# Kernel optimization log

Hardware: AMD Instinct MI355X
Metric: run time of the kernel (lower is better)

## Reference

```python
import jax, jax.numpy as jnp
import numpy as np

L, B, S, D, H, DK, F = 4, 2, 1024, 1024, 16, 64, 4096
EPS = 1e-5  # torch BatchNorm1d default eps


def setup_inputs() -> dict:
    key = jax.random.key(0)
    ks = iter(jax.random.split(key, 64))
    def nrm(shape, scale=0.02):
        return jax.random.normal(next(ks), shape, dtype=jnp.float32) * scale
    inp = {"x": jax.random.normal(next(ks), (B, S, D), dtype=jnp.float32)}
    for i in (1, 2):  # 1 = masked self-attn, 2 = second (unmasked) self-attn
        inp[f"Wq{i}"] = nrm((L, H, D, DK)); inp[f"bq{i}"] = nrm((L, H, DK))
        inp[f"Wk{i}"] = nrm((L, H, D, DK)); inp[f"bk{i}"] = nrm((L, H, DK))
        inp[f"Wv{i}"] = nrm((L, H, D, DK)); inp[f"bv{i}"] = nrm((L, H, DK))
        inp[f"Wo{i}"] = nrm((L, H * DK, D)); inp[f"bo{i}"] = nrm((L, D))
    for i in (1, 2, 3):
        inp[f"g{i}"] = 1.0 + nrm((L, D), 0.1)
        inp[f"be{i}"] = nrm((L, D), 0.1)
    inp["W1"] = nrm((L, D, F)); inp["bf1"] = nrm((L, F))
    inp["W2"] = nrm((L, F, D)); inp["bf2"] = nrm((L, D))
    inp["mask_idx"] = 512
    return inp


def _bn(x, g, b):
    # torch BatchNorm1d(model_dim) on a (B,S,D) tensor: channel axis is 1 (S==D),
    # training mode -> batch statistics over axes (0, 2), biased variance.
    mean = jnp.mean(x, axis=(0, 2), keepdims=True)
    var = jnp.var(x, axis=(0, 2), keepdims=True)
    return g[None, :, None] * (x - mean) * jax.lax.rsqrt(var + EPS) + b[None, :, None]


def _mha(x, Wq, bq, Wk, bk, Wv, bv, Wo, bo, mask_idx):
    # All heads batched into one einsum (same math as the per-head Python loop).
    Bx, Sx, _ = x.shape
    Hh, _, dk = Wq.shape
    q = jnp.einsum('bsd,hdk->bhsk', x, Wq) + bq[None, :, None, :]
    k = jnp.einsum('bsd,hdk->bhsk', x, Wk) + bk[None, :, None, :]
    v = jnp.einsum('bsd,hdk->bhsk', x, Wv) + bv[None, :, None, :]
    s = jnp.einsum('bhsk,bhtk->bhst', q, k) / jnp.sqrt(jnp.asarray(dk, x.dtype))
    if mask_idx is not None:
        # attention_weights[..., mask_idx:] = -inf  (static prefix mask, not causal)
        s = s.at[..., mask_idx:].set(-jnp.inf)
    w = jax.nn.softmax(s, axis=-1)
    a = jnp.einsum('bhst,bhtk->bhsk', w, v)
    a = jnp.transpose(a, (0, 2, 1, 3)).reshape(Bx, Sx, Hh * dk)  # concat heads
    return a @ Wo + bo


def _decoder(x, p, mask_idx):
    def block(h, pl):
        x1 = h + _mha(h, pl['Wq1'], pl['bq1'], pl['Wk1'], pl['bk1'],
                      pl['Wv1'], pl['bv1'], pl['Wo1'], pl['bo1'], mask_idx)
        x1 = _bn(x1, pl['g1'], pl['be1'])
        # note: residual from the block input h, attention over x1 (as in source)
        y = h + _mha(x1, pl['Wq2'], pl['bq2'], pl['Wk2'], pl['bk2'],
                     pl['Wv2'], pl['bv2'], pl['Wo2'], pl['bo2'], None)
        y = _bn(y, pl['g2'], pl['be2'])
        hid = jax.nn.relu(y @ pl['W1'] + pl['bf1'])
        out = x1 + hid @ pl['W2'] + pl['bf2']  # residual from x1 (as in source)
        return _bn(out, pl['g3'], pl['be3']), None
    out, _ = jax.lax.scan(block, x, p)
    return out


def reference(x, Wq1, bq1, Wk1, bk1, Wv1, bv1, Wo1, bo1,
              Wq2, bq2, Wk2, bk2, Wv2, bv2, Wo2, bo2,
              g1, be1, g2, be2, g3, be3, W1, bf1, W2, bf2, mask_idx):
    p = dict(Wq1=Wq1, bq1=bq1, Wk1=Wk1, bk1=bk1, Wv1=Wv1, bv1=bv1, Wo1=Wo1, bo1=bo1,
             Wq2=Wq2, bq2=bq2, Wk2=Wk2, bk2=bk2, Wv2=Wv2, bv2=bv2, Wo2=Wo2, bo2=bo2,
             g1=g1, be1=be1, g2=g2, be2=be2, g3=g3, be3=be3,
             W1=W1, bf1=bf1, W2=W2, bf2=bf2)
    return _decoder(x, p, int(mask_idx))
```

## Files before the change

### kernel.cpp

```cpp
#include <hip/hip_runtime.h>
#include <cstdint>
#include <cstddef>

typedef unsigned short u16;
typedef unsigned int u32;

typedef __bf16 bf16x8 __attribute__((ext_vector_type(8)));
typedef float f32x4 __attribute__((ext_vector_type(4)));

__device__ __forceinline__ float bf2f(u16 v) { return __builtin_bit_cast(float, (u32)v << 16); }
__device__ __forceinline__ u16 f2bf(float f) {
    u32 u = __builtin_bit_cast(u32, f);
    u += 0x7fffu + ((u >> 16) & 1u);
    return (u16)(u >> 16);
}
__device__ __forceinline__ bf16x8 ld8(const u16* p) {
    return __builtin_bit_cast(bf16x8, *(const uint4*)p);
}
__device__ __forceinline__ u32 cvtpk(float lo, float hi) {
    u32 r;
    asm("v_cvt_pk_bf16_f32 %0, %1, %2" : "=v"(r) : "v"(lo), "v"(hi));
    return r;
}
__device__ __forceinline__ void glds16(const u16* g, u16* l) {
    __builtin_amdgcn_global_load_lds((const __attribute__((address_space(1))) void*)g,
                                     (__attribute__((address_space(3))) void*)l, 16, 0, 0);
}

struct B4 { const float* p[4]; };

__global__ __launch_bounds__(256) void conv_f2b(const float* __restrict__ src,
                                                u16* __restrict__ dst)
{
    int idx = blockIdx.x * 256 + threadIdx.x;
    float4 v = ((const float4*)src)[idx];
    uint2 o;
    o.x = (u32)f2bf(v.x) | ((u32)f2bf(v.y) << 16);
    o.y = (u32)f2bf(v.z) | ((u32)f2bf(v.w) << 16);
    ((uint2*)dst)[idx] = o;
}

template <int BM, int BN>
__global__ __launch_bounds__(256) void gemm_bt(
    const u16* __restrict__ A, int lda,
    const u16* __restrict__ Bt, int ldb, int nbs,
    B4 bias,
    const u16* __restrict__ Rres,
    u16* __restrict__ C, int crow, int cbatch, int chead,
    int K, int relu)
{
    constexpr int WM = BM / 2, WN = BN / 2, FM = WM / 16, FN = WN / 16;
    __shared__ __align__(16) u16 Ald[2][BM * 64];
    __shared__ __align__(16) u16 Bld[2][BN * 64];
    const int tid = threadIdx.x;
    const int w = tid >> 6, lane = tid & 63;
    const int qd = lane >> 4, r = lane & 15;
    const int wr = w >> 1, wc = w & 1;
    const int m0 = blockIdx.y * BM, n0 = blockIdx.x * BN;
    const int srow = lane >> 3;
    const int scol = ((lane ^ (lane >> 3)) & 7) * 8;

    auto stage = [&](int buf, int k0) {
#pragma unroll
        for (int ii = 0; ii < BM / 32; ++ii) {
            int rbase = w * (BM / 4) + ii * 8;
            glds16(A + (long)(m0 + rbase + srow) * lda + k0 + scol,
                   &Ald[buf][rbase * 64]);
        }
#pragma unroll
        for (int ii = 0; ii < BN / 32; ++ii) {
            int nbase = w * (BN / 4) + ii * 8;
            int ng = n0 + nbase + srow;
            glds16(Bt + (long)(ng >> 6) * nbs + (long)(ng & 63) * ldb + k0 + scol,
                   &Bld[buf][nbase * 64]);
        }
    };

    f32x4 acc[FM][FN] = {};
    const int nt = K >> 6;

    stage(0, 0);
    __syncthreads();

    for (int t = 0; t < nt; ++t) {
        const int cur = t & 1;
        if (t + 1 < nt) stage(cur ^ 1, (t + 1) << 6);
#pragma unroll
        for (int s = 0; s < 2; ++s) {
            bf16x8 af[FM], bb[FN];
#pragma unroll
            for (int fm = 0; fm < FM; ++fm) {
                int row = wr * WM + fm * 16 + r;
                int blk = ((s << 2) | qd) ^ (r & 7);
                af[fm] = ld8(&Ald[cur][row * 64 + blk * 8]);
            }
#pragma unroll
            for (int fn = 0; fn < FN; ++fn) {
                int row = wc * WN + fn * 16 + r;
                int blk = ((s << 2) | qd) ^ (r & 7);
                bb[fn] = ld8(&Bld[cur][row * 64 + blk * 8]);
            }
#pragma unroll
            for (int fm = 0; fm < FM; ++fm)
#pragma unroll
                for (int fn = 0; fn < FN; ++fn)
                    acc[fm][fn] = __builtin_amdgcn_mfma_f32_16x16x32_bf16(af[fm], bb[fn],
                                                                          acc[fm][fn], 0, 0, 0);
        }
        __syncthreads();
    }

#pragma unroll
    for (int fm = 0; fm < FM; ++fm) {
#pragma unroll
        for (int fn = 0; fn < FN; ++fn) {
            int ng = n0 + wc * WN + fn * 16 + r;
            float bs = bias.p[ng >> 10][ng & 1023];
            int naddr = (ng >> 6) * chead + (ng & 63);
#pragma unroll
            for (int j = 0; j < 4; ++j) {
                int mg = m0 + wr * WM + fm * 16 + qd * 4 + j;
                int caddr = (mg & 1023) * crow + (mg >> 10) * cbatch + naddr;
                float v = acc[fm][fn][j] + bs;
                if (Rres) v += bf2f(Rres[caddr]);
                if (relu) v = fmaxf(v, 0.f);
                C[caddr] = f2bf(v);
            }
        }
    }
}

__global__ __launch_bounds__(256) void vtrans(const u16* __restrict__ src,
                                              u16* __restrict__ dst)
{
    __shared__ u16 tl[32][68];
    const long boff = (long)blockIdx.y * 65536;
    const int s0 = blockIdx.x * 32;
    const int c = threadIdx.x & 63, r4 = threadIdx.x >> 6;
#pragma unroll
    for (int i = 0; i < 8; ++i)
        tl[r4 + 4 * i][c] = src[boff + (long)(s0 + r4 + 4 * i) * 64 + c];
    __syncthreads();
    const int cs = threadIdx.x & 31, rs = threadIdx.x >> 5;
#pragma unroll
    for (int i = 0; i < 8; ++i)
        dst[boff + (long)(rs + 8 * i) * 1024 + s0 + cs] = tl[cs][rs + 8 * i];
}

__global__ __launch_bounds__(256) void attn_kernel(
    const u16* __restrict__ Q, const u16* __restrict__ K,
    const u16* __restrict__ V, u16* __restrict__ O,
    const int* __restrict__ maskp)
{
    __shared__ __align__(16) u16 Kld[2][32 * 64];
    __shared__ __align__(16) u16 Vld[2][64 * 32];
    const int tid = threadIdx.x;
    const int w = tid >> 6, lane = tid & 63;
    const int qd = lane >> 4, r = lane & 15;
    const int bid = blockIdx.x;
    const int xcd = bid & 7, slot = bid >> 3;
    const int bh = xcd + 8 * (slot & 3);
    const int qx = slot >> 2;
    const int b = bh >> 4, h = bh & 15;
    const long base = (long)h * 131072 + (long)b * 65536;
    const int qrow0 = qx * 64 + w * 16;

    int mi = maskp ? *maskp : 1024;
    mi = mi < 0 ? 0 : (mi > 1024 ? 1024 : mi);
    const int ntch = (mi + 31) >> 5;

    const int krho  = tid >> 3;
    const int kperm = ((krho & 12) << 1) | ((krho & 16) >> 2) | (krho & 3);
    const int kg    = (tid & 7) ^ (krho & 7);
    const int vrow = tid >> 2;
    const int vF   = ((vrow & 15) + ((vrow & 15) >> 2)) & 3;
    const int vg   = (tid & 3) ^ vF;

    auto stage = [&](int buf, int c) {
        glds16(K + base + (c * 32 + kperm) * 64 + kg * 8, &Kld[buf][w * 512]);
        glds16(V + base + (long)vrow * 1024 + c * 32 + vg * 8, &Vld[buf][w * 512]);
    };

    bf16x8 aq0 = ld8(&Q[base + (qrow0 + r) * 64 + qd * 8]);
    bf16x8 aq1 = ld8(&Q[base + (qrow0 + r) * 64 + 32 + qd * 8]);

    f32x4 occ[4] = {};
    float sm = 0.f;
    const int rx = r & 7;
    const int kb_a = (qd ^ rx) * 8;
    const int kb_b = ((4 + qd) ^ rx) * 8;
    const int vblk = (qd ^ ((r + (r >> 2)) & 3)) * 8;

    if (ntch > 0) stage(0, 0);
    __syncthreads();

    for (int c = 0; c < ntch; ++c) {
        const int cur = c & 1;
        if (c + 1 < ntch) stage(cur ^ 1, c + 1);

        f32x4 s0 = {}, s1 = {};
        s0 = __builtin_amdgcn_mfma_f32_16x16x32_bf16(
                 ld8(&Kld[cur][r * 64 + kb_a]), aq0, s0, 0, 0, 0);
        s0 = __builtin_amdgcn_mfma_f32_16x16x32_bf16(
                 ld8(&Kld[cur][r * 64 + kb_b]), aq1, s0, 0, 0, 0);
        s1 = __builtin_amdgcn_mfma_f32_16x16x32_bf16(
                 ld8(&Kld[cur][(16 + r) * 64 + kb_a]), aq0, s1, 0, 0, 0);
        s1 = __builtin_amdgcn_mfma_f32_16x16x32_bf16(
                 ld8(&Kld[cur][(16 + r) * 64 + kb_b]), aq1, s1, 0, 0, 0);

        float p0[4], p1[4];
        if ((c + 1) * 32 <= mi) {
#pragma unroll
            for (int j = 0; j < 4; ++j) {
                p0[j] = __expf(fminf(s0[j] * 0.125f, 60.f));
                p1[j] = __expf(fminf(s1[j] * 0.125f, 60.f));
                sm += p0[j] + p1[j];
            }
        } else {
            const int kb8 = c * 32 + qd * 8;
#pragma unroll
            for (int j = 0; j < 4; ++j) {
                p0[j] = (kb8 + j < mi)     ? __expf(fminf(s0[j] * 0.125f, 60.f)) : 0.f;
                p1[j] = (kb8 + 4 + j < mi) ? __expf(fminf(s1[j] * 0.125f, 60.f)) : 0.f;
                sm += p0[j] + p1[j];
            }
        }

        uint4 pk;
        pk.x = cvtpk(p0[0], p0[1]);
        pk.y = cvtpk(p0[2], p0[3]);
        pk.z = cvtpk(p1[0], p1[1]);
        pk.w = cvtpk(p1[2], p1[3]);
        bf16x8 pa = __builtin_bit_cast(bf16x8, pk);

#pragma unroll
        for (int c4 = 0; c4 < 4; ++c4) {
            bf16x8 vv = ld8(&Vld[cur][(c4 * 16 + r) * 32 + vblk]);
            occ[c4] = __builtin_amdgcn_mfma_f32_16x16x32_bf16(pa, vv, occ[c4], 0, 0, 0);
        }
        __syncthreads();
    }

    sm += __shfl_xor(sm, 16);
    sm += __shfl_xor(sm, 32);
    float scale = 1.f / fmaxf(sm, 1e-30f);
    float scj[4];
#pragma unroll
    for (int j = 0; j < 4; ++j) scj[j] = __shfl(scale, qd * 4 + j);

#pragma unroll
    for (int c4 = 0; c4 < 4; ++c4)
#pragma unroll
        for (int j = 0; j < 4; ++j) {
            int row = qrow0 + qd * 4 + j;
            O[(long)(b * 1024 + row) * 1024 + h * 64 + c4 * 16 + r] =
                f2bf(occ[c4][j] * scj[j]);
        }
}

__global__ __launch_bounds__(256) void bn_kernel(
    const u16* __restrict__ X, u16* __restrict__ Y, float* __restrict__ Yf,
    const float* __restrict__ g, const float* __restrict__ be)
{
    __shared__ float red[8];
    const int s = blockIdx.x, tid = threadIdx.x;
    const long b0 = (long)s * 1024, b1 = (long)(1024 + s) * 1024;
    uint2 a0 = *(const uint2*)&X[b0 + tid * 4];
    uint2 a1 = *(const uint2*)&X[b1 + tid * 4];
    float xs[8];
    xs[0] = bf2f((u16)a0.x); xs[1] = bf2f((u16)(a0.x >> 16));
    xs[2] = bf2f((u16)a0.y); xs[3] = bf2f((u16)(a0.y >> 16));
    xs[4] = bf2f((u16)a1.x); xs[5] = bf2f((u16)(a1.x >> 16));
    xs[6] = bf2f((u16)a1.y); xs[7] = bf2f((u16)(a1.y >> 16));
    float s1 = 0.f, s2 = 0.f;
#pragma unroll
    for (int j = 0; j < 8; ++j) { s1 += xs[j]; s2 += xs[j] * xs[j]; }
    for (int o = 32; o; o >>= 1) { s1 += __shfl_down(s1, o); s2 += __shfl_down(s2, o); }
    if ((tid & 63) == 0) { red[(tid >> 6) * 2] = s1; red[(tid >> 6) * 2 + 1] = s2; }
    __syncthreads();
    float S1 = red[0] + red[2] + red[4] + red[6];
    float S2 = red[1] + red[3] + red[5] + red[7];
    float mean = S1 * (1.f / 2048.f);
    float var = fmaxf(S2 * (1.f / 2048.f) - mean * mean, 0.f);
    float gs = g[s] * rsqrtf(var + 1e-5f);
    float bs = be[s];
    float y[8];
#pragma unroll
    for (int j = 0; j < 8; ++j) y[j] = (xs[j] - mean) * gs + bs;
    if (Yf) {
        *(float4*)&Yf[b0 + tid * 4] = make_float4(y[0], y[1], y[2], y[3]);
        *(float4*)&Yf[b1 + tid * 4] = make_float4(y[4], y[5], y[6], y[7]);
    } else {
        *(uint2*)&Y[b0 + tid * 4] = make_uint2(
            (u32)f2bf(y[0]) | ((u32)f2bf(y[1]) << 16),
            (u32)f2bf(y[2]) | ((u32)f2bf(y[3]) << 16));
        *(uint2*)&Y[b1 + tid * 4] = make_uint2(
            (u32)f2bf(y[4]) | ((u32)f2bf(y[5]) << 16),
            (u32)f2bf(y[6]) | ((u32)f2bf(y[7]) << 16));
    }
}

struct TA { const float* s[10]; u16* d[10]; };

__global__ __launch_bounds__(256) void transpose_all(TA ta)
{
    __shared__ u16 tl[32][33];
    int id = blockIdx.x;
    const float* src; u16* dst; int Rr, Cc, tr, tc;
    if (id < 6144) {
        int wgt = id >> 10, rest = id & 1023;
        int head = rest >> 6, tile = rest & 63;
        tr = tile >> 1; tc = tile & 1; Rr = 1024; Cc = 64;
        src = ta.s[wgt] + head * 65536; dst = ta.d[wgt] + head * 65536;
    } else if (id < 8192) {
        int wgt = 6 + ((id - 6144) >> 10), rest = (id - 6144) & 1023;
        tr = rest >> 5; tc = rest & 31; Rr = 1024; Cc = 1024;
        src = ta.s[wgt]; dst = ta.d[wgt];
    } else if (id < 12288) {
        int rest = id - 8192;
        tr = rest >> 7; tc = rest & 127; Rr = 1024; Cc = 4096;
        src = ta.s[8]; dst = ta.d[8];
    } else {
        int rest = id - 12288;
        tr = rest >> 5; tc = rest & 31; Rr = 4096; Cc = 1024;
        src = ta.s[9]; dst = ta.d[9];
    }
    int r0 = tr * 32, c0 = tc * 32;
    int cl = threadIdx.x & 31, rl = threadIdx.x >> 5;
#pragma unroll
    for (int i = 0; i < 4; ++i)
        tl[rl + 8 * i][cl] = f2bf(src[(long)(r0 + rl + 8 * i) * Cc + c0 + cl]);
    __syncthreads();
#pragma unroll
    for (int i = 0; i < 4; ++i)
        dst[(long)(c0 + rl + 8 * i) * Rr + r0 + cl] = tl[cl][rl + 8 * i];
}

extern "C" void kernel_launch(void* const* d_in, const int* in_sizes, int n_in,
                              void* d_out, int out_size, void* d_ws, size_t ws_size,
                              hipStream_t stream)
{
    (void)in_sizes; (void)n_in; (void)out_size;
    const float* x   = (const float*)d_in[0];
    const float* Wq1 = (const float*)d_in[1];
    const float* bq1 = (const float*)d_in[2];
    const float* Wk1 = (const float*)d_in[3];
    const float* bk1 = (const float*)d_in[4];
    const float* Wv1 = (const float*)d_in[5];
    const float* bv1 = (const float*)d_in[6];
    const float* Wo1 = (const float*)d_in[7];
    const float* bo1 = (const float*)d_in[8];
    const float* Wq2 = (const float*)d_in[9];
    const float* bq2 = (const float*)d_in[10];
    const float* Wk2 = (const float*)d_in[11];
    const float* bk2 = (const float*)d_in[12];
    const float* Wv2 = (const float*)d_in[13];
    const float* bv2 = (const float*)d_in[14];
    const float* Wo2 = (const float*)d_in[15];
    const float* bo2 = (const float*)d_in[16];
    const float* g1  = (const float*)d_in[17];
    const float* be1 = (const float*)d_in[18];
    const float* g2  = (const float*)d_in[19];
    const float* be2 = (const float*)d_in[20];
    const float* g3  = (const float*)d_in[21];
    const float* be3 = (const float*)d_in[22];
    const float* W1  = (const float*)d_in[23];
    const float* bf1 = (const float*)d_in[24];
    const float* W2  = (const float*)d_in[25];
    const float* bf2 = (const float*)d_in[26];
    const int* maskp = (const int*)d_in[27];

    u16* ws = (u16*)d_ws;
    const size_t M1 = 1u << 20;
    u16* WT  = ws;
    u16* QKV = ws + 16 * M1;
    u16* Vt  = ws + 22 * M1;
    u16* Ab  = ws + 24 * M1;
    u16* X1  = ws + 26 * M1;
    u16* Yb  = ws + 28 * M1;
    u16* Hb  = ws + 30 * M1;
    u16* HID = ws + 32 * M1;
    u16* T2  = Ab;
    if (ws_size < (size_t)(40 * M1) * sizeof(u16)) return;

    dim3 blk(256);
    dim3 g64(16, 32);
    dim3 gqkv(48, 16);
    dim3 gF1(64, 16);
    dim3 gvt(32, 32);

    conv_f2b<<<dim3(2048), blk, 0, stream>>>(x, Hb);

    for (int l = 0; l < 4; ++l) {
        const u16* hin = Hb;

        TA ta;
        ta.s[0] = Wq1 + (size_t)l * M1;     ta.d[0] = WT + 0 * M1;
        ta.s[1] = Wk1 + (size_t)l * M1;     ta.d[1] = WT + 1 * M1;
        ta.s[2] = Wv1 + (size_t)l * M1;     ta.d[2] = WT + 2 * M1;
        ta.s[3] = Wq2 + (size_t)l * M1;     ta.d[3] = WT + 3 * M1;
        ta.s[4] = Wk2 + (size_t)l * M1;     ta.d[4] = WT + 4 * M1;
        ta.s[5] = Wv2 + (size_t)l * M1;     ta.d[5] = WT + 5 * M1;
        ta.s[6] = Wo1 + (size_t)l * M1;     ta.d[6] = WT + 6 * M1;
        ta.s[7] = Wo2 + (size_t)l * M1;     ta.d[7] = WT + 7 * M1;
        ta.s[8] = W1  + (size_t)l * 4 * M1; ta.d[8] = WT + 8 * M1;
        ta.s[9] = W2  + (size_t)l * 4 * M1; ta.d[9] = WT + 12 * M1;
        transpose_all<<<dim3(16384), blk, 0, stream>>>(ta);

        B4 bQKV1 = {{bq1 + l * 1024, bk1 + l * 1024, bv1 + l * 1024, nullptr}};
        gemm_bt<128, 64><<<gqkv, blk, 0, stream>>>(hin, 1024, WT + 0 * M1, 1024, 65536,
            bQKV1, nullptr, QKV, 64, 65536, 131072, 1024, 0);
        vtrans<<<gvt, blk, 0, stream>>>(QKV + 4 * M1, Vt);
        attn_kernel<<<dim3(512), blk, 0, stream>>>(QKV, QKV + 2 * M1, Vt, Ab, maskp);
        B4 bO1 = {{bo1 + l * 1024, nullptr, nullptr, nullptr}};
        gemm_bt<64, 64><<<g64, blk, 0, stream>>>(Ab, 1024, WT + 6 * M1, 1024, 65536,
            bO1, hin, X1, 1024, 1048576, 64, 1024, 0);
        bn_kernel<<<dim3(1024), blk, 0, stream>>>(X1, X1, nullptr, g1 + l * 1024, be1 + l * 1024);

        B4 bQKV2 = {{bq2 + l * 1024, bk2 + l * 1024, bv2 + l * 1024, nullptr}};
        gemm_bt<128, 64><<<gqkv, blk, 0, stream>>>(X1, 1024, WT + 3 * M1, 1024, 65536,
            bQKV2, nullptr, QKV, 64, 65536, 131072, 1024, 0);
        vtrans<<<gvt, blk, 0, stream>>>(QKV + 4 * M1, Vt);
        attn_kernel<<<dim3(512), blk, 0, stream>>>(QKV, QKV + 2 * M1, Vt, Ab, nullptr);
        B4 bO2 = {{bo2 + l * 1024, nullptr, nullptr, nullptr}};
        gemm_bt<64, 64><<<g64, blk, 0, stream>>>(Ab, 1024, WT + 7 * M1, 1024, 65536,
            bO2, hin, Yb, 1024, 1048576, 64, 1024, 0);
        bn_kernel<<<dim3(1024), blk, 0, stream>>>(Yb, Yb, nullptr, g2 + l * 1024, be2 + l * 1024);

        B4 bF1 = {{bf1 + l * 4096, bf1 + l * 4096 + 1024,
                   bf1 + l * 4096 + 2048, bf1 + l * 4096 + 3072}};
        gemm_bt<128, 64><<<gF1, blk, 0, stream>>>(Yb, 1024, WT + 8 * M1, 1024, 65536,
            bF1, nullptr, HID, 4096, 4194304, 64, 1024, 1);
        B4 bF2 = {{bf2 + l * 1024, nullptr, nullptr, nullptr}};
        gemm_bt<64, 64><<<g64, blk, 0, stream>>>(HID, 4096, WT + 12 * M1, 4096, 262144,
            bF2, X1, T2, 1024, 1048576, 64, 4096, 0);
        bn_kernel<<<dim3(1024), blk, 0, stream>>>(T2, Hb,
            (l == 3) ? (float*)d_out : nullptr, g3 + l * 1024, be3 + l * 1024);
    }
}
```

Measured before the change: 1.142 ms.

## Split-K the FFN down-projection and fuse partial-sum merge into batchnorm

The W2 GEMM (K=4096) is split into four K-slices of 1024, launched as a 3D grid with 4x more blocks, and each slice writes fp32 partials into scratch buffers reused from the weight and QKV workspace. A new bn_merge kernel sums the partials, adds bias and residual, and applies the third batchnorm in one pass, replacing the separate epilogue and bn_kernel. This is meant to raise occupancy for the long-K GEMM, whose 512-block grid leaves CUs underused. In exchange it adds fp32 partial-sum traffic and relies on the aliased scratch regions being dead at that point.

After: 1.132 ms. Within noise of the previous version (-0.9%).

```diff
diff --git a/kernel.cpp b/kernel.cpp
--- a/kernel.cpp
+++ b/kernel.cpp
@@ -28,6 +28,7 @@
 }
 
 struct B4 { const float* p[4]; };
+struct P4 { float* p[4]; };
 
 __global__ __launch_bounds__(256) void conv_f2b(const float* __restrict__ src,
                                                 u16* __restrict__ dst)
@@ -126,6 +127,138 @@
                 if (relu) v = fmaxf(v, 0.f);
                 C[caddr] = f2bf(v);
             }
+        }
+    }
+}
+
+__global__ __launch_bounds__(256) void gemm_splitk(
+    const u16* __restrict__ A, int lda,
+    const u16* __restrict__ Bt, int ldb, int nbs,
+    P4 part)
+{
+    constexpr int BM = 64, BN = 64, WM = 32, WN = 32, FM = 2, FN = 2;
+    __shared__ __align__(16) u16 Ald[2][BM * 64];
+    __shared__ __align__(16) u16 Bld[2][BN * 64];
+    const int tid = threadIdx.x;
+    const int w = tid >> 6, lane = tid & 63;
+    const int qd = lane >> 4, r = lane & 15;
+    const int wr = w >> 1, wc = w & 1;
+    const int m0 = blockIdx.y * BM, n0 = blockIdx.x * BN;
+    const int kbeg = blockIdx.z << 10;
+    float* __restrict__ C = part.p[blockIdx.z];
+    const int srow = lane >> 3;
+    const int scol = ((lane ^ (lane >> 3)) & 7) * 8;
+
+    auto stage = [&](int buf, int k0) {
+#pragma unroll
+        for (int ii = 0; ii < 2; ++ii) {
+            int rbase = w * 16 + ii * 8;
+            glds16(A + (long)(m0 + rbase + srow) * lda + k0 + scol,
+                   &Ald[buf][rbase * 64]);
+        }
+#pragma unroll
+        for (int ii = 0; ii < 2; ++ii) {
+            int nbase = w * 16 + ii * 8;
+            int ng = n0 + nbase + srow;
+            glds16(Bt + (long)(ng >> 6) * nbs + (long)(ng & 63) * ldb + k0 + scol,
+                   &Bld[buf][nbase * 64]);
+        }
+    };
+
+    f32x4 acc[FM][FN] = {};
+
+    stage(0, kbeg);
+    __syncthreads();
+
+    for (int t = 0; t < 16; ++t) {
+        const int cur = t & 1;
+        if (t + 1 < 16) stage(cur ^ 1, kbeg + ((t + 1) << 6));
+#pragma unroll
+        for (int s = 0; s < 2; ++s) {
+            bf16x8 af[FM], bb[FN];
+#pragma unroll
+            for (int fm = 0; fm < FM; ++fm) {
+                int row = wr * WM + fm * 16 + r;
+                int blk = ((s << 2) | qd) ^ (r & 7);
+                af[fm] = ld8(&Ald[cur][row * 64 + blk * 8]);
+            }
+#pragma unroll
+            for (int fn = 0; fn < FN; ++fn) {
+                int row = wc * WN + fn * 16 + r;
+                int blk = ((s << 2) | qd) ^ (r & 7);
+                bb[fn] = ld8(&Bld[cur][row * 64 + blk * 8]);
+            }
+#pragma unroll
+            for (int fm = 0; fm < FM; ++fm)
+#pragma unroll
+                for (int fn = 0; fn < FN; ++fn)
+                    acc[fm][fn] = __builtin_amdgcn_mfma_f32_16x16x32_bf16(af[fm], bb[fn],
+                                                                          acc[fm][fn], 0, 0, 0);
+        }
+        __syncthreads();
+    }
+
+#pragma unroll
+    for (int fm = 0; fm < FM; ++fm) {
+#pragma unroll
+        for (int fn = 0; fn < FN; ++fn) {
+            int ng = n0 + wc * WN + fn * 16 + r;
+#pragma unroll
+            for (int j = 0; j < 4; ++j) {
+                int mg = m0 + wr * WM + fm * 16 + qd * 4 + j;
+                C[(mg & 1023) * 1024 + (mg >> 10) * 1048576 + ng] = acc[fm][fn][j];
+            }
+        }
+    }
+}
+
+__global__ __launch_bounds__(256) void bn_merge(
+    P4 part, const float* __restrict__ bias, const u16* __restrict__ resid,
+    u16* __restrict__ Y, float* __restrict__ Yf,
+    const float* __restrict__ g, const float* __restrict__ be)
+{
+    __shared__ float red[8];
+    const int s = blockIdx.x, tid = threadIdx.x;
+    const int n0 = tid * 4;
+    float xs[8];
+#pragma unroll
+    for (int b = 0; b < 2; ++b) {
+        long off = (long)b * 1048576 + s * 1024 + n0;
+        float4 v0 = *(const float4*)&part.p[0][off];
+        float4 v1 = *(const float4*)&part.p[1][off];
+        float4 v2 = *(const float4*)&part.p[2][off];
+        float4 v3 = *(const float4*)&part.p[3][off];
+        float4 bv = *(const float4*)&bias[n0];
+        uint2 rr = *(const uint2*)&resid[off];
+        xs[b * 4 + 0] = v0.x + v1.x + v2.x + v3.x + bv.x + bf2f((u16)rr.x);
+        xs[b * 4 + 1] = v0.y + v1.y + v2.y + v3.y + bv.y + bf2f((u16)(rr.x >> 16));
+        xs[b * 4 + 2] = v0.z + v1.z + v2.z + v3.z + bv.z + bf2f((u16)rr.y);
+        xs[b * 4 + 3] = v0.w + v1.w + v2.w + v3.w + bv.w + bf2f((u16)(rr.y >> 16));
+    }
+    float s1 = 0.f, s2 = 0.f;
+#pragma unroll
+    for (int j = 0; j < 8; ++j) { s1 += xs[j]; s2 += xs[j] * xs[j]; }
+    for (int o = 32; o; o >>= 1) { s1 += __shfl_down(s1, o); s2 += __shfl_down(s2, o); }
+    if ((tid & 63) == 0) { red[(tid >> 6) * 2] = s1; red[(tid >> 6) * 2 + 1] = s2; }
+    __syncthreads();
+    float S1 = red[0] + red[2] + red[4] + red[6];
+    float S2 = red[1] + red[3] + red[5] + red[7];
+    float mean = S1 * (1.f / 2048.f);
+    float var = fmaxf(S2 * (1.f / 2048.f) - mean * mean, 0.f);
+    float gs = g[s] * rsqrtf(var + 1e-5f);
+    float bs = be[s];
+    float y[8];
+#pragma unroll
+    for (int j = 0; j < 8; ++j) y[j] = (xs[j] - mean) * gs + bs;
+#pragma unroll
+    for (int b = 0; b < 2; ++b) {
+        long off = (long)b * 1048576 + s * 1024 + n0;
+        if (Yf) {
+            *(float4*)&Yf[off] = make_float4(y[b * 4], y[b * 4 + 1], y[b * 4 + 2], y[b * 4 + 3]);
+        } else {
+            *(uint2*)&Y[off] = make_uint2(
+                (u32)f2bf(y[b * 4 + 0]) | ((u32)f2bf(y[b * 4 + 1]) << 16),
+                (u32)f2bf(y[b * 4 + 2]) | ((u32)f2bf(y[b * 4 + 3]) << 16));
         }
     }
 }
@@ -380,13 +513,16 @@
     u16* Yb  = ws + 28 * M1;
     u16* Hb  = ws + 30 * M1;
     u16* HID = ws + 32 * M1;
-    u16* T2  = Ab;
     if (ws_size < (size_t)(40 * M1) * sizeof(u16)) return;
+
+    P4 part = {{(float*)(WT + 0 * M1), (float*)(WT + 4 * M1),
+                (float*)(QKV),         (float*)(QKV + 4 * M1)}};
 
     dim3 blk(256);
     dim3 g64(16, 32);
     dim3 gqkv(48, 16);
     dim3 gF1(64, 16);
+    dim3 gF2(16, 32, 4);
     dim3 gvt(32, 32);
 
     conv_f2b<<<dim3(2048), blk, 0, stream>>>(x, Hb);
@@ -431,10 +567,8 @@
                    bf1 + l * 4096 + 2048, bf1 + l * 4096 + 3072}};
         gemm_bt<128, 64><<<gF1, blk, 0, stream>>>(Yb, 1024, WT + 8 * M1, 1024, 65536,
             bF1, nullptr, HID, 4096, 4194304, 64, 1024, 1);
-        B4 bF2 = {{bf2 + l * 1024, nullptr, nullptr, nullptr}};
-        gemm_bt<64, 64><<<g64, blk, 0, stream>>>(HID, 4096, WT + 12 * M1, 4096, 262144,
-            bF2, X1, T2, 1024, 1048576, 64, 4096, 0);
-        bn_kernel<<<dim3(1024), blk, 0, stream>>>(T2, Hb,
+        gemm_splitk<<<gF2, blk, 0, stream>>>(HID, 4096, WT + 12 * M1, 4096, 262144, part);
+        bn_merge<<<dim3(1024), blk, 0, stream>>>(part, bf2 + l * 1024, X1, Hb,
             (l == 3) ? (float*)d_out : nullptr, g3 + l * 1024, be3 + l * 1024);
     }
 }
```
